# Kernel tuning notes

Measured on AMD Instinct MI355X. Metric: run time of the kernel, lower is better.

Reference implementation:

```python
import jax, jax.numpy as jnp
import numpy as np
from jax import lax

S, B, XD, AD, ZD, K, H = 128, 32, 1024, 8, 4, 3, 50
CN = 32 * 3 * 3
DN = ('NCHW', 'OIHW', 'NCHW')


def setup_inputs():
    key = jax.random.key(0)
    ks = jax.random.split(key, 20)
    g = lambda k, sh, s=0.1: jax.random.normal(k, sh, dtype=jnp.float32) * s
    z = lambda n: jnp.zeros((n,), jnp.float32)
    return {
        'x': jax.random.uniform(ks[0], (S, B, XD), dtype=jnp.float32),
        'eps': jax.random.normal(ks[1], (S, B, AD), dtype=jnp.float32),
        'Wc0': g(ks[2], (32, 1, 3, 3)), 'bc0': z(32),
        'Wc1': g(ks[3], (32, 32, 3, 3)), 'bc1': z(32),
        'Wc2': g(ks[4], (32, 32, 3, 3)), 'bc2': z(32),
        'Wm': g(ks[5], (AD, CN)), 'bm': z(AD),
        'Wlv': g(ks[6], (AD, CN)), 'blv': z(AD),
        'Wd': g(ks[7], (CN, AD)), 'bd': z(CN),
        'Wt0': g(ks[8], (32, 32, 3, 3)), 'bt0': z(32),
        'Wt1': g(ks[9], (32, 32, 3, 3)), 'bt1': z(32),
        'Wt2': g(ks[10], (32, 32, 3, 3)), 'bt2': z(32),
        'Wg': g(ks[11], (32, 1, 1, 1)), 'bg': z(1),
        'A': jnp.tile(jnp.eye(ZD, dtype=jnp.float32)[None], (K, 1, 1)),
        'Bm': g(ks[12], (K, ZD, AD), 0.05),
        'Cm': g(ks[13], (K, AD, ZD), 0.05),
        'a_init': jnp.zeros((1, AD), jnp.float32),
        'W_ih': g(ks[14], (4 * H, AD)), 'W_hh': g(ks[15], (4 * H, H)),
        'b_ih': z(4 * H), 'b_hh': z(4 * H),
        'Wa': g(ks[16], (K, H)), 'ba': z(K),
    }


def _conv(h, W, b):
    y = lax.conv_general_dilated(h, W, (2, 2), 'VALID', dimension_numbers=DN)
    return y + b[None, :, None, None]


def _convT(h, W, b, op):
    # PyTorch ConvTranspose2d(k=3, stride=2, padding=0, output_padding=op)
    Wf = jnp.transpose(jnp.flip(W, (2, 3)), (1, 0, 2, 3))
    pad = (2, 2 + op)
    y = lax.conv_general_dilated(h, Wf, (1, 1), [pad, pad], lhs_dilation=(2, 2), dimension_numbers=DN)
    return y + b[None, :, None, None]


def _forward(x, eps, Wc0, bc0, Wc1, bc1, Wc2, bc2, Wm, bm, Wlv, blv, Wd, bd,
             Wt0, bt0, Wt1, bt1, Wt2, bt2, Wg, bg, A, Bm, Cm, a_init,
             W_ih, W_hh, b_ih, b_hh, Wa, ba):
    relu, sig = jax.nn.relu, jax.nn.sigmoid
    # ---- encode: x -> a ----
    xf = x.reshape(S * B, 1, 32, 32)
    h = relu(_conv(xf, Wc0, bc0))          # (SB,32,15,15)
    h = relu(_conv(h, Wc1, bc1))           # (SB,32,7,7)
    h = relu(_conv(h, Wc2, bc2))           # (SB,32,3,3)
    feat = h.reshape(S, B, CN)
    a_mean = feat @ Wm.T + bm
    a_logvar = sig(feat @ Wlv.T + blv)
    a = a_mean + eps * jnp.exp(0.5 * a_logvar)
    # ---- decode: a -> log_y ----
    d = (a.reshape(S * B, AD) @ Wd.T + bd).reshape(S * B, 32, 3, 3)
    d = relu(_convT(d, Wt0, bt0, 0))       # (SB,32,7,7)
    d = relu(_convT(d, Wt1, bt1, 0))       # (SB,32,15,15)
    d = relu(_convT(d, Wt2, bt2, 1))       # (SB,32,32,32)
    log_y = sig(jnp.einsum('nchw,c->nhw', d, Wg[:, 0, 0, 0]) + bg[0]).reshape(S, B, XD)
    # ---- alpha from a_{t-1} via LSTM ----
    a_tm1 = jnp.concatenate([jnp.broadcast_to(a_init[:, None, :], (1, B, AD)), a[:-1]], 0)
    def lstm_step(carry, xt):
        h_, c_ = carry
        gates = xt @ W_ih.T + b_ih + h_ @ W_hh.T + b_hh
        i, f, gg, o = jnp.split(gates, 4, axis=-1)
        c_ = sig(f) * c_ + sig(i) * jnp.tanh(gg)
        h_ = sig(o) * jnp.tanh(c_)
        return (h_, c_), h_
    _, hs = lax.scan(lstm_step, (jnp.zeros((B, H), jnp.float32), jnp.zeros((B, H), jnp.float32)), a_tm1)
    alpha = jax.nn.softmax(hs @ Wa.T + ba, axis=-1)     # (S,B,K)
    A_mix = jnp.einsum('sbk,kij->sbij', alpha, A)
    B_mix = jnp.einsum('sbk,kij->sbij', alpha, Bm)
    C_mix = jnp.einsum('sbk,kij->sbij', alpha, Cm)
    u = a_tm1
    # ---- Kalman filter ----
    Qm = 0.08 * jnp.eye(ZD, dtype=jnp.float32)
    Rm = 0.03 * jnp.eye(AD, dtype=jnp.float32)
    Iz = jnp.eye(ZD, dtype=jnp.float32)
    mu0 = jnp.zeros((B, ZD), jnp.float32)
    Sigma0 = 20.0 * jnp.tile(Iz[None], (B, 1, 1))
    def filt(carry, xs):
        mu, Sig = carry
        A_t, B_t, C_t, a_t, u_t, first = xs
        mu_p = jnp.einsum('bij,bj->bi', A_t, mu) + jnp.einsum('bij,bj->bi', B_t, u_t)
        Sig_p = A_t @ Sig @ jnp.swapaxes(A_t, 1, 2) + Qm
        mu_p = jnp.where(first, mu0, mu_p)
        Sig_p = jnp.where(first, Sigma0, Sig_p)
        res = a_t - jnp.einsum('bij,bj->bi', C_t, mu_p)
        S_ = C_t @ Sig_p @ jnp.swapaxes(C_t, 1, 2) + Rm
        Kt = Sig_p @ jnp.swapaxes(C_t, 1, 2) @ jnp.linalg.inv(S_)
        mu_f = mu_p + jnp.einsum('bij,bj->bi', Kt, res)
        IKC = Iz - Kt @ C_t
        Sig_f = IKC @ Sig_p @ jnp.swapaxes(IKC, 1, 2) + Kt @ Rm @ jnp.swapaxes(Kt, 1, 2)
        return (mu_f, Sig_f), (mu_p, mu_f, Sig_p, Sig_f)
    first = jnp.arange(S) == 0
    _, (mu_pred, mu_filt, Sig_pred, Sig_filt) = lax.scan(filt, (mu0, Sigma0), (A_mix, B_mix, C_mix, a, u, first))
    # ---- RTS smoother ----
    def smooth(carry, xs):
        mu_s, Sig_s = carry
        Sf, A_n, Sp_n, muf, muf_n = xs
        J = Sf @ jnp.swapaxes(A_n, 1, 2) @ jnp.linalg.inv(Sp_n)
        mu_new = muf + jnp.einsum('bij,bj->bi', J, mu_s - muf_n)
        Sig_new = Sf + J @ (Sig_s - Sp_n) @ jnp.swapaxes(J, 1, 2)
        return (mu_new, Sig_new), (mu_new, Sig_new)
    _, (mu_sm, Sig_sm) = lax.scan(smooth, (mu_filt[-1], Sig_filt[-1]),
                                  (Sig_filt[:-1], A_mix[1:], Sig_pred[1:], mu_filt[:-1], mu_filt[1:]),
                                  reverse=True)
    mu_smooth = jnp.concatenate([mu_sm, mu_filt[-1:]], 0)
    Sigma_smooth = jnp.concatenate([Sig_sm, Sig_filt[-1:]], 0)
    return log_y, a, a_mean, a_logvar, mu_smooth, Sigma_smooth


def reference(x, eps, Wc0, bc0, Wc1, bc1, Wc2, bc2, Wm, bm, Wlv, blv, Wd, bd,
              Wt0, bt0, Wt1, bt1, Wt2, bt2, Wg, bg, A, Bm, Cm, a_init,
              W_ih, W_hh, b_ih, b_hh, Wa, ba):
    return _forward(x, eps, Wc0, bc0, Wc1, bc1, Wc2, bc2, Wm, bm, Wlv, blv, Wd, bd,
                    Wt0, bt0, Wt1, bt1, Wt2, bt2, Wg, bg, A, Bm, Cm, a_init,
                    W_ih, W_hh, b_ih, b_hh, Wa, ba)
```

## Files before the change

kernel.cpp:

```cpp
#include <hip/hip_runtime.h>
#include <math.h>

#define DI __device__ __forceinline__

DI float sigm(float x){ return 1.0f/(1.0f+__expf(-x)); }
DI float tanhx(float x){ float ax=fabsf(x); float e=__expf(2.0f*ax); float t=1.0f-2.0f/(e+1.0f); return copysignf(t,x); }
DI unsigned short f2bf(float x){ unsigned u=__float_as_uint(x); return (unsigned short)((u+0x7fffu+((u>>16)&1u))>>16); }

typedef __attribute__((ext_vector_type(8))) short bf16x8;
typedef __attribute__((ext_vector_type(4))) float f32x4;
#define MFMA16(a,b,c) __builtin_amdgcn_mfma_f32_16x16x32_bf16(a,b,c,0,0,0)

static constexpr int RS  = 296;
static constexpr int RSZ = 9472;
static constexpr int AS  = 40;

static constexpr size_t OFF_A   = 4194304;
static constexpr size_t OFF_AM  = OFF_A   + 32768;
static constexpr size_t OFF_ALV = OFF_AM  + 32768;
static constexpr size_t OFF_MU  = OFF_ALV + 32768;
static constexpr size_t OFF_SG  = OFF_MU  + 16384;

DI float inv4_lane(float Mv, int r, int c){
  int a0=(c==0)?1:0, a1=(c<=1)?2:1, a2=(c<=2)?3:2;
  int b0=(r==0)?1:0, b1=(r<=1)?2:1, b2=(r<=2)?3:2;
  float m00=__shfl(Mv,(a0<<3)|b0,64), m01=__shfl(Mv,(a0<<3)|b1,64), m02=__shfl(Mv,(a0<<3)|b2,64);
  float m10=__shfl(Mv,(a1<<3)|b0,64), m11=__shfl(Mv,(a1<<3)|b1,64), m12=__shfl(Mv,(a1<<3)|b2,64);
  float m20=__shfl(Mv,(a2<<3)|b0,64), m21=__shfl(Mv,(a2<<3)|b1,64), m22=__shfl(Mv,(a2<<3)|b2,64);
  float det3 = m00*(m11*m22-m12*m21) - m01*(m10*m22-m12*m20) + m02*(m10*m21-m11*m20);
  float adj = (((r+c)&1)? -det3 : det3);
  float det=0.f;
  #pragma unroll
  for(int i=0;i<4;i++)
    det += __shfl(Mv,(i<<3),64)*__shfl(adj,i,64);
  return adj*(1.0f/det);
}

DI void inv4_serial(const float* m, float* o){
  float i0 = m[5]*m[10]*m[15]-m[5]*m[11]*m[14]-m[9]*m[6]*m[15]+m[9]*m[7]*m[14]+m[13]*m[6]*m[11]-m[13]*m[7]*m[10];
  float i4 = -m[4]*m[10]*m[15]+m[4]*m[11]*m[14]+m[8]*m[6]*m[15]-m[8]*m[7]*m[14]-m[12]*m[6]*m[11]+m[12]*m[7]*m[10];
  float i8 = m[4]*m[9]*m[15]-m[4]*m[11]*m[13]-m[8]*m[5]*m[15]+m[8]*m[7]*m[13]+m[12]*m[5]*m[11]-m[12]*m[7]*m[9];
  float i12= -m[4]*m[9]*m[14]+m[4]*m[10]*m[13]+m[8]*m[5]*m[14]-m[8]*m[6]*m[13]-m[12]*m[5]*m[10]+m[12]*m[6]*m[9];
  float i1 = -m[1]*m[10]*m[15]+m[1]*m[11]*m[14]+m[9]*m[2]*m[15]-m[9]*m[3]*m[14]-m[13]*m[2]*m[11]+m[13]*m[3]*m[10];
  float i5 = m[0]*m[10]*m[15]-m[0]*m[11]*m[14]-m[8]*m[2]*m[15]+m[8]*m[3]*m[14]+m[12]*m[2]*m[11]-m[12]*m[3]*m[10];
  float i9 = -m[0]*m[9]*m[15]+m[0]*m[11]*m[13]+m[8]*m[1]*m[15]-m[8]*m[3]*m[13]-m[12]*m[1]*m[11]+m[12]*m[3]*m[9];
  float i13= m[0]*m[9]*m[14]-m[0]*m[10]*m[13]-m[8]*m[1]*m[14]+m[8]*m[2]*m[13]+m[12]*m[1]*m[10]-m[12]*m[2]*m[9];
  float i2 = m[1]*m[6]*m[15]-m[1]*m[7]*m[14]-m[5]*m[2]*m[15]+m[5]*m[3]*m[14]+m[13]*m[2]*m[7]-m[13]*m[3]*m[6];
  float i6 = -m[0]*m[6]*m[15]+m[0]*m[7]*m[14]+m[4]*m[2]*m[15]-m[4]*m[3]*m[14]-m[12]*m[2]*m[7]+m[12]*m[3]*m[6];
  float i10= m[0]*m[5]*m[15]-m[0]*m[7]*m[13]-m[4]*m[1]*m[15]+m[4]*m[3]*m[13]+m[12]*m[1]*m[7]-m[12]*m[3]*m[5];
  float i14= -m[0]*m[5]*m[14]+m[0]*m[6]*m[13]+m[4]*m[1]*m[14]-m[4]*m[2]*m[13]-m[12]*m[1]*m[6]+m[12]*m[2]*m[5];
  float i3 = -m[1]*m[6]*m[11]+m[1]*m[7]*m[10]+m[5]*m[2]*m[11]-m[5]*m[3]*m[10]-m[9]*m[2]*m[7]+m[9]*m[3]*m[6];
  float i7 = m[0]*m[6]*m[11]-m[0]*m[7]*m[10]-m[4]*m[2]*m[11]+m[4]*m[3]*m[10]+m[8]*m[2]*m[7]-m[8]*m[3]*m[6];
  float i11= -m[0]*m[5]*m[11]+m[0]*m[7]*m[9]+m[4]*m[1]*m[11]-m[4]*m[3]*m[9]-m[8]*m[1]*m[7]+m[8]*m[3]*m[5];
  float i15= m[0]*m[5]*m[10]-m[0]*m[6]*m[9]-m[4]*m[1]*m[10]+m[4]*m[2]*m[9]+m[8]*m[1]*m[6]-m[8]*m[2]*m[5];
  float rd=1.0f/(m[0]*i0+m[1]*i4+m[2]*i8+m[3]*i12);
  o[0]=i0*rd; o[1]=i1*rd; o[2]=i2*rd; o[3]=i3*rd;
  o[4]=i4*rd; o[5]=i5*rd; o[6]=i6*rd; o[7]=i7*rd;
  o[8]=i8*rd; o[9]=i9*rd; o[10]=i10*rd; o[11]=i11*rd;
  o[12]=i12*rd; o[13]=i13*rd; o[14]=i14*rd; o[15]=i15*rd;
}

__global__ __launch_bounds__(256) void k_prep(
    const float* __restrict__ Wc1, const float* __restrict__ Wc2,
    const float* __restrict__ Wt0, const float* __restrict__ Wt1, const float* __restrict__ Wt2,
    unsigned short* __restrict__ ws16)
{
  int idx = blockIdx.x*256 + threadIdx.x;
  int mat = idx/RSZ, rem = idx%RSZ;
  int co = rem/RS, t = rem%RS;
  float v = 0.f;
  if (t < 288){
    int tap = t>>5, ci = t&31;
    if      (mat==0) v = Wc1[co*288+ci*9+tap];
    else if (mat==1) v = Wc2[co*288+ci*9+tap];
    else if (mat==2) v = Wt0[ci*288+co*9+tap];
    else if (mat==3) v = Wt1[ci*288+co*9+tap];
    else             v = Wt2[ci*288+co*9+tap];
  }
  ws16[idx] = f2bf(v);
}

struct EncSh {
  alignas(16) float img[1024];
  alignas(16) unsigned short h0T[9040];
  alignas(16) unsigned short h1T[2000];
  alignas(16) unsigned short BT1e[9472];
  alignas(16) unsigned short BT2e[9472];
  alignas(16) float feat[288];
};

__global__ __launch_bounds__(256) void k_enc(
    const float* __restrict__ x, const float* __restrict__ eps,
    const float* __restrict__ Wc0, const float* __restrict__ bc0,
    const float* __restrict__ bc1, const float* __restrict__ bc2,
    const float* __restrict__ Wm, const float* __restrict__ bm,
    const float* __restrict__ Wlv, const float* __restrict__ blv,
    const unsigned short* __restrict__ ws16,
    float* __restrict__ out)
{
  __shared__ EncSh E;
  const int n = blockIdx.x, tid = threadIdx.x;
  const int lane = tid & 63, wave = tid >> 6, g = lane >> 4, c15 = lane & 15;

  for (int i=tid;i<1024;i+=256) E.img[i]=x[(size_t)n*1024+i];
  {
    uint4* dst=(uint4*)E.BT1e;
    const uint4* src=(const uint4*)ws16;
    for (int i=tid;i<2368;i+=256) dst[i]=src[i];
  }
  if (tid<32){ E.h0T[225*AS+tid]=0; E.h1T[49*AS+tid]=0; }
  __syncthreads();

  for (int i=tid;i<7200;i+=256){
    int co=i&31, p=i>>5, oy=p/15, ox=p%15;
    float acc=bc0[co];
    const float* wp=Wc0+co*9;
    int base=2*oy*32+2*ox;
    #pragma unroll
    for(int ky=0;ky<3;ky++)
      #pragma unroll
      for(int kx=0;kx<3;kx++)
        acc += E.img[base+ky*32+kx]*wp[ky*3+kx];
    E.h0T[p*AS+co]=f2bf(fmaxf(acc,0.0f));
  }
  __syncthreads();

  {
    const int mt=wave;
    const int oy=mt*2+(c15>>3), ox=c15&7;
    f32x4 acc0={0.f,0.f,0.f,0.f}, acc1={0.f,0.f,0.f,0.f};
    #pragma unroll 1
    for (int ky=0;ky<3;ky++){
      #pragma unroll
      for (int kx=0;kx<3;kx++){
        int iy=2*oy+ky, ix=2*ox+kx;
        int pix=(iy<15&&ix<15)?(iy*15+ix):225;
        bf16x8 af=*(const bf16x8*)&E.h0T[pix*AS+g*8];
        int tap=ky*3+kx;
        bf16x8 b0=*(const bf16x8*)&E.BT1e[c15*RS+tap*32+g*8];
        bf16x8 b1=*(const bf16x8*)&E.BT1e[(c15+16)*RS+tap*32+g*8];
        acc0=MFMA16(af,b0,acc0);
        acc1=MFMA16(af,b1,acc1);
      }
    }
    float bA=bc1[c15], bB=bc1[c15+16];
    #pragma unroll
    for (int r=0;r<4;r++){
      int p16=g*4+r, oy2=mt*2+(p16>>3), ox2=p16&7;
      if (oy2<7 && ox2<7){
        E.h1T[(oy2*7+ox2)*AS+c15]   =f2bf(fmaxf(acc0[r]+bA,0.f));
        E.h1T[(oy2*7+ox2)*AS+c15+16]=f2bf(fmaxf(acc1[r]+bB,0.f));
      }
    }
  }
  __syncthreads();

  if (wave<2){
    const int nt=wave;
    const int valid=(c15<9);
    const int oy=c15/3, ox=c15-oy*3;
    f32x4 acc={0.f,0.f,0.f,0.f};
    #pragma unroll 1
    for (int ky=0;ky<3;ky++){
      #pragma unroll
      for (int kx=0;kx<3;kx++){
        int pix=valid?((2*oy+ky)*7+(2*ox+kx)):49;
        bf16x8 af=*(const bf16x8*)&E.h1T[pix*AS+g*8];
        int tap=ky*3+kx;
        bf16x8 bfr=*(const bf16x8*)&E.BT2e[(nt*16+c15)*RS+tap*32+g*8];
        acc=MFMA16(af,bfr,acc);
      }
    }
    float bb=bc2[nt*16+c15];
    #pragma unroll
    for (int r=0;r<4;r++){
      int p16=g*4+r;
      if (p16<9) E.feat[(nt*16+c15)*9+p16]=fmaxf(acc[r]+bb,0.f);
    }
  }
  __syncthreads();

  if (tid<64){
    const int j=tid>>3, kk=tid&7;
    float s1=0.f,s2=0.f;
    const float* wm=Wm+j*288;
    const float* wl=Wlv+j*288;
    #pragma unroll 6
    for(int m=kk*36;m<kk*36+36;m++){ float f=E.feat[m]; s1+=f*wm[m]; s2+=f*wl[m]; }
    #pragma unroll
    for(int d=4;d>0;d>>=1){ s1+=__shfl_down(s1,d,64); s2+=__shfl_down(s2,d,64); }
    if(kk==0){
      size_t o=(size_t)n*8+j;
      float am=s1+bm[j];
      float lv=sigm(s2+blv[j]);
      float av=am+eps[o]*__expf(0.5f*lv);
      out[OFF_AM+o]=am;
      out[OFF_ALV+o]=lv;
      out[OFF_A+o]=av;
    }
  }
}

struct DecSh {
  alignas(16) float aa[8];
  alignas(16) unsigned short d0T[400];
  alignas(16) unsigned short t0T[2000];
  alignas(16) unsigned short t1T[9040];
  alignas(16) unsigned short BT0[9472];
  alignas(16) unsigned short BT1[9472];
  alignas(16) unsigned short BT2[9472];
};
struct SeqSh {
  alignas(16) float a_loc[1024];
  alignas(16) float a0[8];
  alignas(16) float h[56];
  float gates[200];
  float logit[4];
  float alpha[384];
  float muf[512];
  float Sigf[2048];
  float Sigp[2048];
  float Jb[2048];
  float Amat[48];
  float Bmat[96];
  float Cmat[96];
  float gram[96];
  float zk[1536];
  float Buk[1536];
  float mca[2048];
  float zbu[1024];
};
union MainSh { DecSh d; SeqSh q; };

__global__ __launch_bounds__(512) void k_main(
    const float* __restrict__ Wd, const float* __restrict__ bd,
    const float* __restrict__ bt0, const float* __restrict__ bt1, const float* __restrict__ bt2,
    const float* __restrict__ Wg, const float* __restrict__ bgp,
    const float* __restrict__ Ag, const float* __restrict__ Bg, const float* __restrict__ Cg,
    const float* __restrict__ a_init,
    const float* __restrict__ W_ih, const float* __restrict__ W_hh,
    const float* __restrict__ b_ih, const float* __restrict__ b_hh,
    const float* __restrict__ Wa, const float* __restrict__ ba,
    const unsigned short* __restrict__ ws16,
    float* __restrict__ out)
{
  __shared__ MainSh sh;
  const int tid=threadIdx.x;
  const float* aglob = out + OFF_A;

  if (blockIdx.x < 32){
    if (tid>=320) return;
    __builtin_amdgcn_s_setprio(1);
    SeqSh& Q = sh.q;
    const int b=blockIdx.x;
    for (int i=tid;i<1024;i+=320){ int s=i>>3, j=i&7; Q.a_loc[i]=aglob[((size_t)s*32+b)*8+j]; }
    if (tid<8)  Q.a0[tid]=a_init[tid];
    if (tid<56) Q.h[tid]=0.f;
    for (int i=tid;i<48;i+=320) Q.Amat[i]=Ag[i];
    for (int i=tid;i<96;i+=320){ Q.Bmat[i]=Bg[i]; Q.Cmat[i]=Cg[i]; }

    const int gr = tid-64;
    float wr[52], wi[8], bsum=0.f, creg=0.f;
    if (tid>=64 && tid<264){
      #pragma unroll
      for(int k=0;k<50;k++) wr[k]=W_hh[gr*50+k];
      wr[50]=0.f; wr[51]=0.f;
      #pragma unroll
      for(int j=0;j<8;j++) wi[j]=W_ih[gr*8+j];
      bsum=b_ih[gr]+b_hh[gr];
    }
    float wl[52]; float bl=0.f;
    if (tid>=264 && tid<267){
      #pragma unroll
      for(int k=0;k<50;k++) wl[k]=Wa[(tid-264)*50+k];
      wl[50]=0.f; wl[51]=0.f;
      bl=ba[tid-264];
    }
    const int r=tid>>3, c=tid&7;
    bool aid=false;
    if (tid<64){
      int ok=1;
      if (r<4&&c<4){
        float d=(r==c)?1.f:0.f;
        ok=(Ag[r*4+c]==d)&&(Ag[16+r*4+c]==d)&&(Ag[32+r*4+c]==d);
      }
      aid=(bool)__all(ok);
    }
    __syncthreads();
    if (tid<96){
      int which=tid>>4, e=tid&15, i2=e>>2, j2=e&3;
      float s2=0.f;
      if (which<3){
        const float* C=&Q.Cmat[which*32];
        #pragma unroll
        for(int m=0;m<8;m++) s2+=C[m*4+i2]*C[m*4+j2];
      } else {
        int k2=(which==5)?1:0, l2=(which==3)?1:2;
        const float* Ck=&Q.Cmat[k2*32];
        const float* Cl=&Q.Cmat[l2*32];
        #pragma unroll
        for(int m=0;m<8;m++) s2+=Ck[m*4+i2]*Cl[m*4+j2]+Cl[m*4+i2]*Ck[m*4+j2];
      }
      Q.gram[tid]=s2;
    }
    for (int idx=tid; idx<1536; idx+=320){
      int s=idx/12, r2=idx-s*12, k=r2>>2, i=r2&3;
      const float* Crow=&Q.Cmat[k*32];
      const float* Brow=&Q.Bmat[k*32+i*8];
      const float* av=&Q.a_loc[s*8];
      const float* uv=(s==0)?Q.a0:&Q.a_loc[(s-1)*8];
      float z2=0.f, bu=0.f;
      #pragma unroll
      for(int m=0;m<8;m++){ z2+=Crow[m*4+i]*av[m]; bu+=Brow[m]*uv[m]; }
      Q.zk[idx]=z2; Q.Buk[idx]=bu;
    }
    __syncthreads();

    for (int s=0;s<128;s++){
      if (tid>=64 && tid<264){
        const float* ap=(s==0)?Q.a0:(Q.a_loc+(s-1)*8);
        float4 av0=*(const float4*)ap, av1=*(const float4*)(ap+4);
        float aA=bsum+av0.x*wi[0]+av0.y*wi[1]+av0.z*wi[2]+av0.w*wi[3]
                     +av1.x*wi[4]+av1.y*wi[5]+av1.z*wi[6]+av1.w*wi[7];
        float aB=0.f,aC=0.f,aD=0.f;
        #pragma unroll
        for(int q=0;q<13;q++){
          float4 hv=*(const float4*)&Q.h[4*q];
          aA+=hv.x*wr[4*q]; aB+=hv.y*wr[4*q+1]; aC+=hv.z*wr[4*q+2]; aD+=hv.w*wr[4*q+3];
        }
        Q.gates[gr]=(aA+aB)+(aC+aD);
      } else if (tid>=264 && tid<267){
        if (s>0){
          float aA=bl,aB=0.f,aC=0.f,aD=0.f;
          #pragma unroll
          for(int q=0;q<13;q++){
            float4 hv=*(const float4*)&Q.h[4*q];
            aA+=hv.x*wl[4*q]; aB+=hv.y*wl[4*q+1]; aC+=hv.z*wl[4*q+2]; aD+=hv.w*wl[4*q+3];
          }
          Q.logit[tid-264]=(aA+aB)+(aC+aD);
        }
      }
      __syncthreads();
      if (tid>=64 && tid<114){
        int j=gr;
        float ig=sigm(Q.gates[j]);
        float fg=sigm(Q.gates[50+j]);
        float gg=tanhx(Q.gates[100+j]);
        float og=sigm(Q.gates[150+j]);
        creg=fg*creg+ig*gg;
        Q.h[j]=og*tanhx(creg);
      } else if (tid>=114 && tid<117 && s>0){
        int j=tid-114;
        float l0=Q.logit[0], l1=Q.logit[1], l2=Q.logit[2];
        float mx=fmaxf(l0,fmaxf(l1,l2));
        float e0=__expf(l0-mx), e1=__expf(l1-mx), e2=__expf(l2-mx);
        float lj=(j==0)?l0:((j==1)?l1:l2);
        Q.alpha[(s-1)*3+j]=__expf(lj-mx)/(e0+e1+e2);
      }
      __syncthreads();
    }
    if (tid>=264 && tid<267){
      float aA=bl,aB=0.f,aC=0.f,aD=0.f;
      #pragma unroll
      for(int q=0;q<13;q++){
        float4 hv=*(const float4*)&Q.h[4*q];
        aA+=hv.x*wl[4*q]; aB+=hv.y*wl[4*q+1]; aC+=hv.z*wl[4*q+2]; aD+=hv.w*wl[4*q+3];
      }
      Q.logit[tid-264]=(aA+aB)+(aC+aD);
    }
    __syncthreads();
    if (tid<3){
      int j=tid;
      float l0=Q.logit[0], l1=Q.logit[1], l2=Q.logit[2];
      float mx=fmaxf(l0,fmaxf(l1,l2));
      float e0=__expf(l0-mx), e1=__expf(l1-mx), e2=__expf(l2-mx);
      float lj=(j==0)?l0:((j==1)?l1:l2);
      Q.alpha[127*3+j]=__expf(lj-mx)/(e0+e1+e2);
    }
    __syncthreads();
    for (int idx=tid; idx<2048; idx+=320){
      int s=idx>>4, e=idx&15;
      float al0=Q.alpha[s*3+0], al1=Q.alpha[s*3+1], al2=Q.alpha[s*3+2];
      Q.mca[idx]= al0*al0*Q.gram[e]    + al1*al1*Q.gram[16+e] + al2*al2*Q.gram[32+e]
                + al0*al1*Q.gram[48+e] + al0*al2*Q.gram[64+e] + al1*al2*Q.gram[80+e];
    }
    for (int idx=tid; idx<1024; idx+=320){
      int s=idx>>3, t=idx&7;
      float al0=Q.alpha[s*3+0], al1=Q.alpha[s*3+1], al2=Q.alpha[s*3+2];
      if (t<4) Q.zbu[idx]=al0*Q.zk[s*12+t]+al1*Q.zk[s*12+4+t]+al2*Q.zk[s*12+8+t];
      else {
        int i=t-4;
        Q.zbu[idx]=al0*Q.Buk[s*12+i]+al1*Q.Buk[s*12+4+i]+al2*Q.Buk[s*12+8+i];
      }
    }
    __syncthreads();
    if (tid<64){
      const bool act=(r<4&&c<4);
      const int cc=c&3, rr4=r&3;
      float mu0=0.f,mu1=0.f,mu2=0.f,mu3=0.f, Sg=0.f;
      for (int s3=0;s3<128;s3++){
        const float* mrow=&Q.mca[s3*16+cc*4];
        float mr0=mrow[0], mr1=mrow[1], mr2=mrow[2], mr3=mrow[3];
        float mc0=Q.mca[s3*16+cc], mc1=Q.mca[s3*16+4+cc], mc2=Q.mca[s3*16+8+cc], mc3=Q.mca[s3*16+12+cc];
        float zc=Q.zbu[s3*8+cc];
        float bu0=Q.zbu[s3*8+4], bu1=Q.zbu[s3*8+5], bu2=Q.zbu[s3*8+6], bu3=Q.zbu[s3*8+7];
        float mp0,mp1,mp2,mp3, Sp;
        if (aid){
          mp0=mu0+bu0; mp1=mu1+bu1; mp2=mu2+bu2; mp3=mu3+bu3;
          Sp=Sg+((r==c)?0.08f:0.f);
        } else {
          float al0=Q.alpha[s3*3+0], al1=Q.alpha[s3*3+1], al2=Q.alpha[s3*3+2];
          int e2=(rr4<<2)|cc;
          float At=al0*Q.Amat[e2]+al1*Q.Amat[16+e2]+al2*Q.Amat[32+e2];
          float mcc=(c==0)?mu0:((c==1)?mu1:((c==2)?mu2:((c==3)?mu3:0.f)));
          float qv=(c<4)?At*mcc:0.f;
          qv+=__shfl_xor(qv,1,64); qv+=__shfl_xor(qv,2,64);
          float bur=(rr4==0)?bu0:((rr4==1)?bu1:((rr4==2)?bu2:bu3));
          float rowv=qv+bur;
          mp0=__shfl(rowv,0,64); mp1=__shfl(rowv,8,64); mp2=__shfl(rowv,16,64); mp3=__shfl(rowv,24,64);
          float T=0.f;
          #pragma unroll
          for(int k=0;k<4;k++) T+=__shfl(At,(r<<3)|k,64)*__shfl(Sg,(k<<3)|c,64);
          float sp=0.f;
          #pragma unroll
          for(int k=0;k<4;k++) sp+=__shfl(T,(r<<3)|k,64)*__shfl(At,(c<<3)|k,64);
          Sp=sp+((r==c)?0.08f:0.f);
        }
        if (s3==0){ mp0=0.f;mp1=0.f;mp2=0.f;mp3=0.f; Sp=(r==c)?20.f:0.f; }
        if (act) Q.Sigp[s3*16+rr4*4+cc]=Sp;
        float wc=zc-(mr0*mp0+mr1*mp1+mr2*mp2+mr3*mp3);
        float gv=(r==c)?1.f:0.f;
        gv+=__shfl(Sp,(r<<3)|0,64)*mc0*(1.0f/0.03f);
        gv+=__shfl(Sp,(r<<3)|1,64)*mc1*(1.0f/0.03f);
        gv+=__shfl(Sp,(r<<3)|2,64)*mc2*(1.0f/0.03f);
        gv+=__shfl(Sp,(r<<3)|3,64)*mc3*(1.0f/0.03f);
        float Gi=inv4_lane(gv,r,c);
        float Sf=0.f;
        #pragma unroll
        for(int k=0;k<4;k++) Sf+=__shfl(Gi,(r<<3)|k,64)*__shfl(Sp,(k<<3)|c,64);
        if (act) Q.Sigf[s3*16+rr4*4+cc]=Sf;
        float p=(c<4)?Sf*wc:0.f;
        p+=__shfl_xor(p,1,64); p+=__shfl_xor(p,2,64);
        float mpr=(r==0)?mp0:((r==1)?mp1:((r==2)?mp2:mp3));
        float mufr=mpr+p*(1.0f/0.03f);
        if (r<4&&c==0) Q.muf[s3*4+r]=mufr;
        mu0=__shfl(mufr,0,64); mu1=__shfl(mufr,8,64); mu2=__shfl(mufr,16,64); mu3=__shfl(mufr,24,64);
        Sg=Sf;
      }
    }
    __syncthreads();
    if (tid<127){
      const int n2=tid;
      float al0=Q.alpha[(n2+1)*3+0], al1=Q.alpha[(n2+1)*3+1], al2=Q.alpha[(n2+1)*3+2];
      float An[16], Sp[16], Spi[16], Sf[16], T[16];
      #pragma unroll
      for(int k=0;k<16;k++){
        An[k]=al0*Q.Amat[k]+al1*Q.Amat[16+k]+al2*Q.Amat[32+k];
        Sp[k]=Q.Sigp[(n2+1)*16+k];
        Sf[k]=Q.Sigf[n2*16+k];
      }
      inv4_serial(Sp,Spi);
      #pragma unroll
      for(int r2=0;r2<4;r2++)
        #pragma unroll
        for(int c2=0;c2<4;c2++){
          float s2=0.f;
          #pragma unroll
          for(int k=0;k<4;k++) s2+=Sf[r2*4+k]*An[c2*4+k];
          T[r2*4+c2]=s2;
        }
      #pragma unroll
      for(int r2=0;r2<4;r2++)
        #pragma unroll
        for(int c2=0;c2<4;c2++){
          float s2=0.f;
          #pragma unroll
          for(int k=0;k<4;k++) s2+=T[r2*4+k]*Spi[k*4+c2];
          Q.Jb[n2*16+r2*4+c2]=s2;
        }
    }
    __syncthreads();
    if (tid<64){
      const bool act=(r<4&&c<4);
      if (r<4&&c==0) out[OFF_MU+((size_t)127*32+b)*4+r]=Q.muf[127*4+r];
      if (act)       out[OFF_SG+((size_t)127*32+b)*16+r*4+c]=Q.Sigf[127*16+r*4+c];
      float ms0=Q.muf[508], ms1=Q.muf[509], ms2=Q.muf[510], ms3=Q.muf[511];
      float Ss=act?Q.Sigf[127*16+r*4+c]:0.f;
      for (int n2=126;n2>=0;n2--){
        float Jv =act?Q.Jb[n2*16+r*4+c]:0.f;
        float Sfv=act?Q.Sigf[n2*16+r*4+c]:0.f;
        float Spn=act?Q.Sigp[(n2+1)*16+r*4+c]:0.f;
        float Dv=Ss-Spn;
        float T2=0.f;
        #pragma unroll
        for(int k=0;k<4;k++) T2+=__shfl(Jv,(r<<3)|k,64)*__shfl(Dv,(k<<3)|c,64);
        float Sn=Sfv;
        #pragma unroll
        for(int k=0;k<4;k++) Sn+=__shfl(T2,(r<<3)|k,64)*__shfl(Jv,(c<<3)|k,64);
        float msc=(c==0)?ms0:((c==1)?ms1:((c==2)?ms2:ms3));
        float dmc=(c<4)?(msc-Q.muf[(n2+1)*4+(c&3)]):0.f;
        float p=Jv*dmc;
        p+=__shfl_xor(p,1,64); p+=__shfl_xor(p,2,64);
        float mun=Q.muf[n2*4+(r&3)]+p;
        if (r<4&&c==0) out[OFF_MU+((size_t)n2*32+b)*4+r]=mun;
        if (act)       out[OFF_SG+((size_t)n2*32+b)*16+r*4+c]=Sn;
        ms0=__shfl(mun,0,64); ms1=__shfl(mun,8,64); ms2=__shfl(mun,16,64); ms3=__shfl(mun,24,64);
        Ss=Sn;
      }
    }
    return;
  }

  DecSh& D = sh.d;
  const int n = blockIdx.x - 32;
  const int lane = tid & 63, wave = tid >> 6, g = lane >> 4, c15 = lane & 15;

  if (tid<8) D.aa[tid]=aglob[(size_t)n*8+tid];
  {
    uint4* dst=(uint4*)D.BT0;
    const uint4* src=(const uint4*)(ws16 + 2*RSZ);
    for (int i=tid;i<3552;i+=512) dst[i]=src[i];
  }
  if (tid<32){ D.d0T[9*AS+tid]=0; D.t0T[49*AS+tid]=0; D.t1T[225*AS+tid]=0; }
  __syncthreads();
  if (tid<288){
    float acc=bd[tid];
    #pragma unroll
    for(int j=0;j<8;j++) acc+=D.aa[j]*Wd[tid*8+j];
    D.d0T[(tid%9)*AS+(tid/9)]=f2bf(acc);
  }
  __syncthreads();
  {
    const int mt=wave>>1, nt=wave&1;
    const int pa=mt*16+c15;
    const int oh=pa/7, ow=pa%7;
    const bool pv=(pa<49);
    f32x4 acc={0.f,0.f,0.f,0.f};
    #pragma unroll 1
    for (int kh=0;kh<3;kh++){
      int th=oh-kh;
      bool vh=pv && th>=0 && !(th&1) && th<=4;
      int ihb=(th>>1)*3;
      #pragma unroll
      for (int kw=0;kw<3;kw++){
        int tw=ow-kw;
        bool v=vh && tw>=0 && !(tw&1) && tw<=4;
        int pix=v?(ihb+(tw>>1)):9;
        bf16x8 af=*(const bf16x8*)&D.d0T[pix*AS+g*8];
        int tap=kh*3+kw;
        bf16x8 bb=*(const bf16x8*)&D.BT0[(nt*16+c15)*RS+tap*32+g*8];
        acc=MFMA16(af,bb,acc);
      }
    }
    float bz=bt0[nt*16+c15];
    #pragma unroll
    for (int r=0;r<4;r++){
      int pc=mt*16+g*4+r;
      if (pc<49) D.t0T[pc*AS+nt*16+c15]=f2bf(fmaxf(acc[r]+bz,0.f));
    }
  }
  __syncthreads();
  {
    float bA=bt1[c15], bB=bt1[c15+16];
    #pragma unroll 1
    for (int u2=0;u2<2;u2++){
      int unit=wave+u2*8;
      int cls=unit>>2, mt=unit&3;
      int ph=cls>>1, pw=cls&1;
      int ii=mt*2+(c15>>3), jj=c15&7;
      f32x4 acc0={0.f,0.f,0.f,0.f}, acc1={0.f,0.f,0.f,0.f};
      #pragma unroll 1
      for (int kh=ph;kh<3;kh+=2){
        int ih=ii-(kh>>1);
        #pragma unroll
        for (int kw=pw;kw<3;kw+=2){
          int iw=jj-(kw>>1);
          int pix=(ih>=0&&ih<7&&iw>=0&&iw<7)?(ih*7+iw):49;
          bf16x8 af=*(const bf16x8*)&D.t0T[pix*AS+g*8];
          int tap=kh*3+kw;
          bf16x8 b0=*(const bf16x8*)&D.BT1[c15*RS+tap*32+g*8];
          bf16x8 b1=*(const bf16x8*)&D.BT1[(c15+16)*RS+tap*32+g*8];
          acc0=MFMA16(af,b0,acc0);
          acc1=MFMA16(af,b1,acc1);
        }
      }
      #pragma unroll
      for (int r=0;r<4;r++){
        int p16=g*4+r;
        int iio=mt*2+(p16>>3), jjo=p16&7;
        int oh=2*iio+ph, ow=2*jjo+pw;
        if (oh<15 && ow<15){
          D.t1T[(oh*15+ow)*AS+c15]   =f2bf(fmaxf(acc0[r]+bA,0.f));
          D.t1T[(oh*15+ow)*AS+c15+16]=f2bf(fmaxf(acc1[r]+bB,0.f));
        }
      }
    }
  }
  __syncthreads();
  {
    float bt2a=bt2[c15], bt2b=bt2[c15+16], wga=Wg[c15], wgb=Wg[c15+16], bgv=bgp[0];
    #pragma unroll 1
    for (int u2=0;u2<2;u2++){
      int ii=wave+u2*8;
      #pragma unroll 1
      for (int cls=0;cls<4;cls++){
        int ph=cls>>1, pw=cls&1;
        f32x4 acc0={0.f,0.f,0.f,0.f}, acc1={0.f,0.f,0.f,0.f};
        #pragma unroll 1
        for (int kh=ph;kh<3;kh+=2){
          int ih=ii-(kh>>1);
          if (ih<0||ih>14) continue;
          #pragma unroll
          for (int kw=pw;kw<3;kw+=2){
            int iw=c15-(kw>>1);
            int pix=(iw>=0&&iw<15)?(ih*15+iw):225;
            bf16x8 af=*(const bf16x8*)&D.t1T[pix*AS+g*8];
            int tap=kh*3+kw;
            bf16x8 b0=*(const bf16x8*)&D.BT2[c15*RS+tap*32+g*8];
            bf16x8 b1=*(const bf16x8*)&D.BT2[(c15+16)*RS+tap*32+g*8];
            acc0=MFMA16(af,b0,acc0);
            acc1=MFMA16(af,b1,acc1);
          }
        }
        int oh=2*ii+ph;
        float s0=fmaxf(acc0[0]+bt2a,0.f)*wga+fmaxf(acc1[0]+bt2b,0.f)*wgb;
        float s1=fmaxf(acc0[1]+bt2a,0.f)*wga+fmaxf(acc1[1]+bt2b,0.f)*wgb;
        float s2=fmaxf(acc0[2]+bt2a,0.f)*wga+fmaxf(acc1[2]+bt2b,0.f)*wgb;
        float s3=fmaxf(acc0[3]+bt2a,0.f)*wga+fmaxf(acc1[3]+bt2b,0.f)*wgb;
        #pragma unroll
        for (int d=1;d<16;d<<=1){
          s0+=__shfl_xor(s0,d,64); s1+=__shfl_xor(s1,d,64);
          s2+=__shfl_xor(s2,d,64); s3+=__shfl_xor(s3,d,64);
        }
        if (c15==0){
          size_t ob=(size_t)n*1024+(size_t)oh*32+pw;
          out[ob+2*(g*4+0)]=sigm(s0+bgv);
          out[ob+2*(g*4+1)]=sigm(s1+bgv);
          out[ob+2*(g*4+2)]=sigm(s2+bgv);
          out[ob+2*(g*4+3)]=sigm(s3+bgv);
        }
      }
    }
  }
}

extern "C" void kernel_launch(void* const* d_in, const int* in_sizes, int n_in,
                              void* d_out, int out_size, void* d_ws, size_t ws_size,
                              hipStream_t stream)
{
  const float* x    =(const float*)d_in[0];
  const float* eps  =(const float*)d_in[1];
  const float* Wc0  =(const float*)d_in[2];
  const float* bc0  =(const float*)d_in[3];
  const float* Wc1  =(const float*)d_in[4];
  const float* bc1  =(const float*)d_in[5];
  const float* Wc2  =(const float*)d_in[6];
  const float* bc2  =(const float*)d_in[7];
  const float* Wm   =(const float*)d_in[8];
  const float* bm   =(const float*)d_in[9];
  const float* Wlv  =(const float*)d_in[10];
  const float* blv  =(const float*)d_in[11];
  const float* Wd   =(const float*)d_in[12];
  const float* bd   =(const float*)d_in[13];
  const float* Wt0  =(const float*)d_in[14];
  const float* bt0  =(const float*)d_in[15];
  const float* Wt1  =(const float*)d_in[16];
  const float* bt1  =(const float*)d_in[17];
  const float* Wt2  =(const float*)d_in[18];
  const float* bt2  =(const float*)d_in[19];
  const float* Wg   =(const float*)d_in[20];
  const float* bg   =(const float*)d_in[21];
  const float* A    =(const float*)d_in[22];
  const float* Bm   =(const float*)d_in[23];
  const float* Cm   =(const float*)d_in[24];
  const float* a0   =(const float*)d_in[25];
  const float* W_ih =(const float*)d_in[26];
  const float* W_hh =(const float*)d_in[27];
  const float* b_ih =(const float*)d_in[28];
  const float* b_hh =(const float*)d_in[29];
  const float* Wa   =(const float*)d_in[30];
  const float* ba   =(const float*)d_in[31];
  float* out=(float*)d_out;
  unsigned short* ws16=(unsigned short*)d_ws;

  k_prep<<<185,256,0,stream>>>(Wc1,Wc2,Wt0,Wt1,Wt2,ws16);
  k_enc<<<4096,256,0,stream>>>(x,eps,Wc0,bc0,bc1,bc2,Wm,bm,Wlv,blv,ws16,out);
  k_main<<<4128,512,0,stream>>>(Wd,bd,bt0,bt1,bt2,Wg,bg,A,Bm,Cm,a0,
                                W_ih,W_hh,b_ih,b_hh,Wa,ba,ws16,out);
}
```

Before: 312.9 us.

## Run LSTM recurrence in a single wave with bf16 shared weights

```diff
diff --git a/kernel.cpp b/kernel.cpp
--- a/kernel.cpp
+++ b/kernel.cpp
@@ -6,6 +6,8 @@
 DI float sigm(float x){ return 1.0f/(1.0f+__expf(-x)); }
 DI float tanhx(float x){ float ax=fabsf(x); float e=__expf(2.0f*ax); float t=1.0f-2.0f/(e+1.0f); return copysignf(t,x); }
 DI unsigned short f2bf(float x){ unsigned u=__float_as_uint(x); return (unsigned short)((u+0x7fffu+((u>>16)&1u))>>16); }
+DI float bflo(unsigned u){ return __uint_as_float(u<<16); }
+DI float bfhi(unsigned u){ return __uint_as_float(u&0xffff0000u); }
 
 typedef __attribute__((ext_vector_type(8))) short bf16x8;
 typedef __attribute__((ext_vector_type(4))) float f32x4;
@@ -213,9 +215,8 @@
 struct SeqSh {
   alignas(16) float a_loc[1024];
   alignas(16) float a0[8];
-  alignas(16) float h[56];
-  float gates[200];
-  float logit[4];
+  alignas(16) float xvec[64];
+  alignas(16) unsigned short Wbf[13056];
   float alpha[384];
   float muf[512];
   float Sigf[2048];
@@ -225,8 +226,6 @@
   float Bmat[96];
   float Cmat[96];
   float gram[96];
-  float zk[1536];
-  float Buk[1536];
   float mca[2048];
   float zbu[1024];
 };
@@ -249,32 +248,24 @@
   const float* aglob = out + OFF_A;
 
   if (blockIdx.x < 32){
-    if (tid>=320) return;
     __builtin_amdgcn_s_setprio(1);
     SeqSh& Q = sh.q;
     const int b=blockIdx.x;
-    for (int i=tid;i<1024;i+=320){ int s=i>>3, j=i&7; Q.a_loc[i]=aglob[((size_t)s*32+b)*8+j]; }
+    for (int i=tid;i<1024;i+=512){ int s=i>>3, j=i&7; Q.a_loc[i]=aglob[((size_t)s*32+b)*8+j]; }
     if (tid<8)  Q.a0[tid]=a_init[tid];
-    if (tid<56) Q.h[tid]=0.f;
-    for (int i=tid;i<48;i+=320) Q.Amat[i]=Ag[i];
-    for (int i=tid;i<96;i+=320){ Q.Bmat[i]=Bg[i]; Q.Cmat[i]=Cg[i]; }
-
-    const int gr = tid-64;
-    float wr[52], wi[8], bsum=0.f, creg=0.f;
-    if (tid>=64 && tid<264){
-      #pragma unroll
-      for(int k=0;k<50;k++) wr[k]=W_hh[gr*50+k];
-      wr[50]=0.f; wr[51]=0.f;
-      #pragma unroll
-      for(int j=0;j<8;j++) wi[j]=W_ih[gr*8+j];
-      bsum=b_ih[gr]+b_hh[gr];
-    }
-    float wl[52]; float bl=0.f;
-    if (tid>=264 && tid<267){
-      #pragma unroll
-      for(int k=0;k<50;k++) wl[k]=Wa[(tid-264)*50+k];
-      wl[50]=0.f; wl[51]=0.f;
-      bl=ba[tid-264];
+    if (tid<64) Q.xvec[tid]=(tid<8)?a_init[tid]:0.f;
+    for (int i=tid;i<48;i+=512) Q.Amat[i]=Ag[i];
+    for (int i=tid;i<96;i+=512){ Q.Bmat[i]=Bg[i]; Q.Cmat[i]=Cg[i]; }
+    for (int idx=tid; idx<13056; idx+=512){
+      int row=idx>>6, k=idx&63;
+      float v=0.f;
+      if (row<200){
+        if (k<8) v=W_ih[row*8+k];
+        else if (k<58) v=W_hh[row*50+(k-8)];
+      } else if (row<203){
+        if (k>=8 && k<58) v=Wa[(row-200)*50+(k-8)];
+      }
+      Q.Wbf[idx]=f2bf(v);
     }
     const int r=tid>>3, c=tid&7;
     bool aid=false;
@@ -303,95 +294,111 @@
       }
       Q.gram[tid]=s2;
     }
-    for (int idx=tid; idx<1536; idx+=320){
-      int s=idx/12, r2=idx-s*12, k=r2>>2, i=r2&3;
-      const float* Crow=&Q.Cmat[k*32];
-      const float* Brow=&Q.Bmat[k*32+i*8];
-      const float* av=&Q.a_loc[s*8];
-      const float* uv=(s==0)?Q.a0:&Q.a_loc[(s-1)*8];
-      float z2=0.f, bu=0.f;
-      #pragma unroll
-      for(int m=0;m<8;m++){ z2+=Crow[m*4+i]*av[m]; bu+=Brow[m]*uv[m]; }
-      Q.zk[idx]=z2; Q.Buk[idx]=bu;
-    }
     __syncthreads();
 
-    for (int s=0;s<128;s++){
-      if (tid>=64 && tid<264){
-        const float* ap=(s==0)?Q.a0:(Q.a_loc+(s-1)*8);
-        float4 av0=*(const float4*)ap, av1=*(const float4*)(ap+4);
-        float aA=bsum+av0.x*wi[0]+av0.y*wi[1]+av0.z*wi[2]+av0.w*wi[3]
-                     +av1.x*wi[4]+av1.y*wi[5]+av1.z*wi[6]+av1.w*wi[7];
-        float aB=0.f,aC=0.f,aD=0.f;
-        #pragma unroll
-        for(int q=0;q<13;q++){
-          float4 hv=*(const float4*)&Q.h[4*q];
-          aA+=hv.x*wr[4*q]; aB+=hv.y*wr[4*q+1]; aC+=hv.z*wr[4*q+2]; aD+=hv.w*wr[4*q+3];
-        }
-        Q.gates[gr]=(aA+aB)+(aC+aD);
-      } else if (tid>=264 && tid<267){
-        if (s>0){
-          float aA=bl,aB=0.f,aC=0.f,aD=0.f;
-          #pragma unroll
-          for(int q=0;q<13;q++){
-            float4 hv=*(const float4*)&Q.h[4*q];
-            aA+=hv.x*wl[4*q]; aB+=hv.y*wl[4*q+1]; aC+=hv.z*wl[4*q+2]; aD+=hv.w*wl[4*q+3];
+    if (tid<64){
+      const int j=tid;
+      const bool gate=(j<50), lg=(j>=50 && j<53), act54=(j<54);
+      int r0=(j<50)?j:((j<54)?(150+j):203);
+      int r1=(j<50)?(50+j):203;
+      int r2=(j<50)?(100+j):203;
+      int r3=(j<50)?(150+j):203;
+      float b0=0.f,b1=0.f,b2=0.f,b3=0.f;
+      if (gate){
+        b0=b_ih[j]+b_hh[j]; b1=b_ih[50+j]+b_hh[50+j];
+        b2=b_ih[100+j]+b_hh[100+j]; b3=b_ih[150+j]+b_hh[150+j];
+      } else if (lg) b0=ba[j-50];
+      const unsigned short* w0=&Q.Wbf[r0*64];
+      const unsigned short* w1=&Q.Wbf[r1*64];
+      const unsigned short* w2=&Q.Wbf[r2*64];
+      const unsigned short* w3=&Q.Wbf[r3*64];
+      float creg=0.f;
+      for (int s=0;s<128;s++){
+        if (act54){
+          float acc0=b0,acc1=b1,acc2=b2,acc3=b3;
+          #pragma unroll
+          for(int q=0;q<8;q++){
+            float4 xa=*(const float4*)&Q.xvec[8*q];
+            float4 xb=*(const float4*)&Q.xvec[8*q+4];
+            uint4 u0=*(const uint4*)&w0[8*q];
+            uint4 u1=*(const uint4*)&w1[8*q];
+            uint4 u2=*(const uint4*)&w2[8*q];
+            uint4 u3=*(const uint4*)&w3[8*q];
+            acc0+=bflo(u0.x)*xa.x+bfhi(u0.x)*xa.y+bflo(u0.y)*xa.z+bfhi(u0.y)*xa.w
+                 +bflo(u0.z)*xb.x+bfhi(u0.z)*xb.y+bflo(u0.w)*xb.z+bfhi(u0.w)*xb.w;
+            acc1+=bflo(u1.x)*xa.x+bfhi(u1.x)*xa.y+bflo(u1.y)*xa.z+bfhi(u1.y)*xa.w
+                 +bflo(u1.z)*xb.x+bfhi(u1.z)*xb.y+bflo(u1.w)*xb.z+bfhi(u1.w)*xb.w;
+            acc2+=bflo(u2.x)*xa.x+bfhi(u2.x)*xa.y+bflo(u2.y)*xa.z+bfhi(u2.y)*xa.w
+                 +bflo(u2.z)*xb.x+bfhi(u2.z)*xb.y+bflo(u2.w)*xb.z+bfhi(u2.w)*xb.w;
+            acc3+=bflo(u3.x)*xa.x+bfhi(u3.x)*xa.y+bflo(u3.y)*xa.z+bfhi(u3.y)*xa.w
+                 +bflo(u3.z)*xb.x+bfhi(u3.z)*xb.y+bflo(u3.w)*xb.z+bfhi(u3.w)*xb.w;
           }
-          Q.logit[tid-264]=(aA+aB)+(aC+aD);
-        }
-      }
-      __syncthreads();
-      if (tid>=64 && tid<114){
-        int j=gr;
-        float ig=sigm(Q.gates[j]);
-        float fg=sigm(Q.gates[50+j]);
-        float gg=tanhx(Q.gates[100+j]);
-        float og=sigm(Q.gates[150+j]);
-        creg=fg*creg+ig*gg;
-        Q.h[j]=og*tanhx(creg);
-      } else if (tid>=114 && tid<117 && s>0){
-        int j=tid-114;
-        float l0=Q.logit[0], l1=Q.logit[1], l2=Q.logit[2];
+          if (gate){
+            float ig=sigm(acc0), fg=sigm(acc1), gg=tanhx(acc2), og=sigm(acc3);
+            creg=fg*creg+ig*gg;
+            Q.xvec[8+j]=og*tanhx(creg);
+          }
+          if (j<8) Q.xvec[j]=Q.a_loc[s*8+j];
+          if (lg && s>0){
+            float l0=__shfl(acc0,50,64), l1=__shfl(acc0,51,64), l2=__shfl(acc0,52,64);
+            float mx=fmaxf(l0,fmaxf(l1,l2));
+            float e0=__expf(l0-mx), e1=__expf(l1-mx), e2=__expf(l2-mx);
+            float me=(j==50)?l0:((j==51)?l1:l2);
+            Q.alpha[(s-1)*3+(j-50)]=__expf(me-mx)/(e0+e1+e2);
+          }
+        }
+      }
+      if (lg){
+        float acc0=b0;
+        #pragma unroll
+        for(int q=0;q<8;q++){
+          float4 xa=*(const float4*)&Q.xvec[8*q];
+          float4 xb=*(const float4*)&Q.xvec[8*q+4];
+          uint4 u0=*(const uint4*)&w0[8*q];
+          acc0+=bflo(u0.x)*xa.x+bfhi(u0.x)*xa.y+bflo(u0.y)*xa.z+bfhi(u0.y)*xa.w
+               +bflo(u0.z)*xb.x+bfhi(u0.z)*xb.y+bflo(u0.w)*xb.z+bfhi(u0.w)*xb.w;
+        }
+        float l0=__shfl(acc0,50,64), l1=__shfl(acc0,51,64), l2=__shfl(acc0,52,64);
         float mx=fmaxf(l0,fmaxf(l1,l2));
         float e0=__expf(l0-mx), e1=__expf(l1-mx), e2=__expf(l2-mx);
-        float lj=(j==0)?l0:((j==1)?l1:l2);
-        Q.alpha[(s-1)*3+j]=__expf(lj-mx)/(e0+e1+e2);
-      }
-      __syncthreads();
-    }
-    if (tid>=264 && tid<267){
-      float aA=bl,aB=0.f,aC=0.f,aD=0.f;
-      #pragma unroll
-      for(int q=0;q<13;q++){
-        float4 hv=*(const float4*)&Q.h[4*q];
-        aA+=hv.x*wl[4*q]; aB+=hv.y*wl[4*q+1]; aC+=hv.z*wl[4*q+2]; aD+=hv.w*wl[4*q+3];
-      }
-      Q.logit[tid-264]=(aA+aB)+(aC+aD);
+        float me=(j==50)?l0:((j==51)?l1:l2);
+        Q.alpha[127*3+(j-50)]=__expf(me-mx)/(e0+e1+e2);
+      }
     }
     __syncthreads();
-    if (tid<3){
-      int j=tid;
-      float l0=Q.logit[0], l1=Q.logit[1], l2=Q.logit[2];
-      float mx=fmaxf(l0,fmaxf(l1,l2));
-      float e0=__expf(l0-mx), e1=__expf(l1-mx), e2=__expf(l2-mx);
-      float lj=(j==0)?l0:((j==1)?l1:l2);
-      Q.alpha[127*3+j]=__expf(lj-mx)/(e0+e1+e2);
-    }
-    __syncthreads();
-    for (int idx=tid; idx<2048; idx+=320){
+    for (int idx=tid; idx<2048; idx+=512){
       int s=idx>>4, e=idx&15;
       float al0=Q.alpha[s*3+0], al1=Q.alpha[s*3+1], al2=Q.alpha[s*3+2];
       Q.mca[idx]= al0*al0*Q.gram[e]    + al1*al1*Q.gram[16+e] + al2*al2*Q.gram[32+e]
                 + al0*al1*Q.gram[48+e] + al0*al2*Q.gram[64+e] + al1*al2*Q.gram[80+e];
     }
-    for (int idx=tid; idx<1024; idx+=320){
+    for (int idx=tid; idx<1024; idx+=512){
       int s=idx>>3, t=idx&7;
       float al0=Q.alpha[s*3+0], al1=Q.alpha[s*3+1], al2=Q.alpha[s*3+2];
-      if (t<4) Q.zbu[idx]=al0*Q.zk[s*12+t]+al1*Q.zk[s*12+4+t]+al2*Q.zk[s*12+8+t];
-      else {
+      float res=0.f;
+      if (t<4){
+        const float* av=&Q.a_loc[s*8];
+        #pragma unroll
+        for(int k=0;k<3;k++){
+          float d=0.f;
+          const float* C=&Q.Cmat[k*32];
+          #pragma unroll
+          for(int m=0;m<8;m++) d+=C[m*4+t]*av[m];
+          res+=((k==0)?al0:((k==1)?al1:al2))*d;
+        }
+      } else {
         int i=t-4;
-        Q.zbu[idx]=al0*Q.Buk[s*12+i]+al1*Q.Buk[s*12+4+i]+al2*Q.Buk[s*12+8+i];
-      }
+        const float* uv=(s==0)?Q.a0:&Q.a_loc[(s-1)*8];
+        #pragma unroll
+        for(int k=0;k<3;k++){
+          float d=0.f;
+          const float* B=&Q.Bmat[k*32+i*8];
+          #pragma unroll
+          for(int m=0;m<8;m++) d+=B[m]*uv[m];
+          res+=((k==0)?al0:((k==1)?al1:al2))*d;
+        }
+      }
+      Q.zbu[idx]=res;
     }
     __syncthreads();
     if (tid<64){
@@ -554,9 +561,9 @@
     }
     float bz=bt0[nt*16+c15];
     #pragma unroll
-    for (int r=0;r<4;r++){
-      int pc=mt*16+g*4+r;
-      if (pc<49) D.t0T[pc*AS+nt*16+c15]=f2bf(fmaxf(acc[r]+bz,0.f));
+    for (int r2=0;r2<4;r2++){
+      int pc=mt*16+g*4+r2;
+      if (pc<49) D.t0T[pc*AS+nt*16+c15]=f2bf(fmaxf(acc[r2]+bz,0.f));
     }
   }
   __syncthreads();
@@ -585,13 +592,13 @@
         }
       }
       #pragma unroll
-      for (int r=0;r<4;r++){
-        int p16=g*4+r;
+      for (int r2=0;r2<4;r2++){
+        int p16=g*4+r2;
         int iio=mt*2+(p16>>3), jjo=p16&7;
         int oh=2*iio+ph, ow=2*jjo+pw;
         if (oh<15 && ow<15){
-          D.t1T[(oh*15+ow)*AS+c15]   =f2bf(fmaxf(acc0[r]+bA,0.f));
-          D.t1T[(oh*15+ow)*AS+c15+16]=f2bf(fmaxf(acc1[r]+bB,0.f));
+          D.t1T[(oh*15+ow)*AS+c15]   =f2bf(fmaxf(acc0[r2]+bA,0.f));
+          D.t1T[(oh*15+ow)*AS+c15+16]=f2bf(fmaxf(acc1[r2]+bB,0.f));
         }
       }
     }
```

New measurement: 423.7 us. +35.4%, slower.
